# Performance work log

Hardware: AMD Instinct MI355X
Metric: run time of the kernel (lower is better)

Reference implementation:

```python
import jax, jax.numpy as jnp
import numpy as np

N_RAYS, MAX_S, N_VOX, EMB, HID, L_VIEW = 8192, 64, 100000, 32, 128, 4


def view_pe(d):
    # NeRF positional encoding of view dirs: [N,3] -> [N, 3 + 6*L_VIEW]
    freqs = 2.0 ** jnp.arange(L_VIEW, dtype=d.dtype)
    ang = (d[..., None] * freqs).reshape(*d.shape[:-1], -1)  # [N, 3*L]
    return jnp.concatenate([d, jnp.sin(ang), jnp.cos(ang)], -1)


def setup_inputs() -> dict:
    key = jax.random.key(0)
    ks = jax.random.split(key, 16)
    rays_d = jax.random.normal(ks[0], (N_RAYS, 3), dtype=jnp.float32)
    rays_d = rays_d / jnp.linalg.norm(rays_d, axis=-1, keepdims=True)
    pts = jax.random.uniform(ks[1], (N_RAYS, MAX_S, 3), dtype=jnp.float32)
    t_vals = jnp.sort(jax.random.uniform(ks[2], (N_RAYS, MAX_S), dtype=jnp.float32) * 4.0, axis=-1)
    dists = jnp.concatenate([t_vals[:, 1:] - t_vals[:, :-1], jnp.full((N_RAYS, 1), 0.05, jnp.float32)], -1)
    # ragged per-ray sample counts -> -1 padded p2v_idx (as produced by the voxel point sampler)
    counts = jax.random.randint(ks[3], (N_RAYS,), 1, MAX_S + 1)
    ray_hits = jax.random.bernoulli(ks[4], 0.9, (N_RAYS,))
    valid = (jnp.arange(MAX_S)[None, :] < counts[:, None]) & ray_hits[:, None]
    idx = jax.random.randint(ks[5], (N_RAYS, MAX_S), 0, N_VOX)
    p2v_idx = jnp.where(valid, idx, -1).astype(jnp.int32)

    def lin(k, i, o):
        return jax.random.normal(k, (i, o), dtype=jnp.float32) * np.float32(1.0 / np.sqrt(i))

    return dict(
        rays_d=rays_d, pts=pts, t_vals=t_vals, dists=dists,
        p2v_idx=p2v_idx, ray_hits=ray_hits,
        vox_emb=jax.random.normal(ks[6], (N_VOX, EMB), dtype=jnp.float32) * 0.1,
        Wpts=lin(ks[7], 3, EMB),
        W1=lin(ks[8], EMB, HID), b1=jnp.zeros((HID,), jnp.float32),
        W2=lin(ks[9], HID, HID), b2=jnp.zeros((HID,), jnp.float32),
        Wsig=lin(ks[10], HID, 1), bsig=jnp.zeros((1,), jnp.float32),
        Wfeat=lin(ks[11], HID, HID), bfeat=jnp.zeros((HID,), jnp.float32),
        Wc1=lin(ks[12], HID + 3 + 6 * L_VIEW, 64), bc1=jnp.zeros((64,), jnp.float32),
        Wc2=lin(ks[13], 64, 3), bc2=jnp.zeros((3,), jnp.float32),
    )


def reference(rays_d, pts, t_vals, dists, vox_emb, Wpts, W1, b1, W2, b2,
              Wsig, bsig, Wfeat, bfeat, Wc1, bc1, Wc2, bc2, p2v_idx, ray_hits):
    mask = p2v_idx >= 0                                   # [N,S] valid samples (mask_pts)
    idx = jnp.where(mask, p2v_idx, 0)
    # voxel_embedder: per-point voxel embedding gather + positional lift
    ve = vox_emb[idx] + pts @ Wpts                        # [N,S,EMB]
    h = jax.nn.relu(ve @ W1 + b1)
    h = jax.nn.relu(h @ W2 + b2)                          # [N,S,HID]
    sigma = (h @ Wsig + bsig)[..., 0]                     # [N,S]
    feat = h @ Wfeat + bfeat                              # [N,S,HID]
    vemb = view_pe(rays_d)                                # [N,27]
    vemb = jnp.broadcast_to(vemb[:, None, :], (feat.shape[0], feat.shape[1], vemb.shape[-1]))
    c = jax.nn.relu(jnp.concatenate([feat, vemb], -1) @ Wc1 + bc1)
    rgb_raw = c @ Wc2 + bc2                               # [N,S,3]
    # masked_scatter semantics: invalid slots are 0 before the min_color remap
    rgb = (jnp.where(mask[..., None], rgb_raw, 0.0) + 1.0) * 0.5   # min_color = -1
    free_energy = jnp.where(mask, jax.nn.relu(sigma) * dists, 0.0)  # [N,S]
    # volumetric_rendering(with_dist=True)
    shifted = jnp.concatenate([jnp.zeros_like(free_energy[:, :1]), free_energy[:, :-1]], -1)
    T = jnp.exp(-jnp.cumsum(shifted, -1))
    weights = (1.0 - jnp.exp(-free_energy)) * T           # [N,S]
    comp_rgb = jnp.einsum('ns,nsc->nc', weights, rgb)     # [N,3]
    acc = weights.sum(-1)                                 # [N]
    depth = (weights * t_vals).sum(-1)
    disp = 1.0 / jnp.maximum(1e-10, depth / jnp.maximum(acc, 1e-10))
    # fill_in for missed rays (white_bkgd=False -> fill with 0)
    comp_rgb = jnp.where(ray_hits[:, None], comp_rgb, 0.0)
    disp = jnp.where(ray_hits, disp, 0.0)
    acc = jnp.where(ray_hits, acc, 0.0)
    return comp_rgb, disp, acc
```

## Files before the change

kernel.cpp:

```cpp
#include <hip/hip_runtime.h>
#include <stdint.h>


#define NRAYS 8192
#define MAXS  64
#define EMB   32
#define HID   128
#define NPE   27
#define CH    64
#define NPTS  (NRAYS * MAXS)
#define RCAP  16384

#define WS_WCOMB  0
#define WS_WPE    (WS_WCOMB + HID*CH)
#define WS_BCOMB  (WS_WPE + 32*CH)
#define WS_CCINIT (WS_BCOMB + CH)
#define WS_COUNTS (WS_CCINIT + NRAYS*CH)
#define WS_OFFS   (WS_COUNTS + NRAYS)
#define WS_TOTAL  (WS_OFFS + NRAYS)
#define WS_RCNT   (WS_TOTAL + 1)
#define WS_LIST   (WS_TOTAL + 4)
#define WS_PTOUT  (WS_LIST + NPTS)
#define WS_FRAGS  (WS_PTOUT + 4*NPTS)
#define WS_RLIST  (WS_FRAGS + 56*2*64*4)
#define WS_PTSC   (WS_RLIST + RCAP)

typedef __attribute__((ext_vector_type(8))) short bf16x8;
typedef __attribute__((ext_vector_type(4))) float f32x4;
union FI { int i[4]; int4 v; bf16x8 f; };

#define MFMA16(a, b, c) __builtin_amdgcn_mfma_f32_16x16x32_bf16(a, b, c, 0, 0, 0)

__device__ __forceinline__ f32x4 mfma3(bf16x8 ah, bf16x8 al, bf16x8 bh, bf16x8 bl,
                                       f32x4 c) {
  c = MFMA16(al, bh, c);
  c = MFMA16(ah, bl, c);
  c = MFMA16(ah, bh, c);
  return c;
}

__device__ __forceinline__ void split8(const float* x, bf16x8& hi, bf16x8& lo) {
  FI H, L;
#pragma unroll
  for (int r = 0; r < 4; ++r) {
    unsigned u0 = __float_as_uint(x[2 * r]);
    unsigned u1 = __float_as_uint(x[2 * r + 1]);
    unsigned h0 = u0 & 0xffff0000u, h1 = u1 & 0xffff0000u;
    unsigned l0 = __float_as_uint(x[2 * r] - __uint_as_float(h0));
    unsigned l1 = __float_as_uint(x[2 * r + 1] - __uint_as_float(h1));
    H.i[r] = (int)((h0 >> 16) | (h1 & 0xffff0000u));
    L.i[r] = (int)((l0 >> 16) | (l1 & 0xffff0000u));
  }
  hi = H.f; lo = L.f;
}

__device__ __forceinline__ int packword(float v) {
  unsigned u = __float_as_uint(v);
  unsigned hb = u & 0xffff0000u;
  unsigned lb = __float_as_uint(v - __uint_as_float(hb));
  return (int)((u >> 16) | (lb & 0xffff0000u));
}

__device__ __forceinline__ void unpack8(const int* w, bf16x8& hi, bf16x8& lo) {
  FI H, L;
#pragma unroll
  for (int r = 0; r < 4; ++r) {
    unsigned w0 = (unsigned)w[2 * r], w1 = (unsigned)w[2 * r + 1];
    H.i[r] = (int)((w0 & 0xffffu) | (w1 << 16));
    L.i[r] = (int)((w0 >> 16) | (w1 & 0xffff0000u));
  }
  hi = H.f; lo = L.f;
}

__global__ __launch_bounds__(256) void prep_kernel(
    const float* __restrict__ Wfeat, const float* __restrict__ bfeat,
    const float* __restrict__ Wc1, const float* __restrict__ bc1,
    float* __restrict__ ws) {
  int idx = blockIdx.x * 256 + threadIdx.x;
  if (idx < HID * CH) {
    int m = idx >> 6, j = idx & 63;
    float s = 0.f;
    for (int f = 0; f < HID; ++f) s = fmaf(Wfeat[m * HID + f], Wc1[f * CH + j], s);
    ws[WS_WCOMB + idx] = s;
    return;
  }
  idx -= HID * CH;
  if (idx < 32 * CH) {
    int v = idx >> 6, j = idx & 63;
    ws[WS_WPE + idx] = (v < NPE) ? Wc1[(HID + v) * CH + j] : 0.f;
    return;
  }
  idx -= 32 * CH;
  if (idx < CH) {
    float s = bc1[idx];
    for (int f = 0; f < HID; ++f) s = fmaf(bfeat[f], Wc1[f * CH + idx], s);
    ws[WS_BCOMB + idx] = s;
    return;
  }
  idx -= CH;
  if (idx < 2) ((int*)(ws + WS_TOTAL))[idx] = 0;
}

__global__ __launch_bounds__(256) void prep2_kernel(
    const float* __restrict__ W1, const float* __restrict__ W2,
    float* __restrict__ ws) {
  int t = blockIdx.x * 256 + threadIdx.x;
  if (t >= 56 * 64) return;
  const int fid = t >> 6, lane = t & 63;
  const int n16 = lane & 15, quad = lane >> 4;
  float x[8];
  if (fid < 8) {
    const int n = fid * 16 + n16, k0 = quad * 8;
#pragma unroll
    for (int j = 0; j < 8; ++j) x[j] = W1[(k0 + j) * HID + n];
  } else if (fid < 40) {
    const int f = fid - 8, nt = f >> 2, s = f & 3;
    const int n = nt * 16 + n16, k0 = s * 32 + quad * 8;
#pragma unroll
    for (int j = 0; j < 8; ++j) x[j] = W2[(k0 + j) * HID + n];
  } else {
    const int f = fid - 40, nt = f >> 2, s = f & 3;
    const int n = nt * 16 + n16, k0 = s * 32 + quad * 8;
#pragma unroll
    for (int j = 0; j < 8; ++j) x[j] = ws[WS_WCOMB + (k0 + j) * CH + n];
  }
  FI H, L;
#pragma unroll
  for (int r = 0; r < 4; ++r) {
    unsigned u0 = __float_as_uint(x[2 * r]);
    unsigned u1 = __float_as_uint(x[2 * r + 1]);
    unsigned h0 = u0 & 0xffff0000u, h1 = u1 & 0xffff0000u;
    unsigned l0 = __float_as_uint(x[2 * r] - __uint_as_float(h0));
    unsigned l1 = __float_as_uint(x[2 * r + 1] - __uint_as_float(h1));
    H.i[r] = (int)((h0 >> 16) | (h1 & 0xffff0000u));
    L.i[r] = (int)((l0 >> 16) | (l1 & 0xffff0000u));
  }
  int4* o = (int4*)(ws + WS_FRAGS);
  o[(fid * 2 + 0) * 64 + lane] = H.v;
  o[(fid * 2 + 1) * 64 + lane] = L.v;
}

__global__ __launch_bounds__(256) void count_pe_kernel(
    const float* __restrict__ rays_d, const int* __restrict__ p2v,
    float* __restrict__ ws) {
  const int tid = threadIdx.x;
  const int ray = blockIdx.x * 4 + (tid >> 6);
  const int lane = tid & 63;
  const int v = p2v[ray * MAXS + lane];
  const unsigned long long ball = __ballot(v >= 0);
  if (lane == 0) ((int*)(ws + WS_COUNTS))[ray] = __popcll(ball);

  const float d0 = rays_d[ray * 3 + 0];
  const float d1 = rays_d[ray * 3 + 1];
  const float d2 = rays_d[ray * 3 + 2];
  float vemb[NPE];
  vemb[0] = d0; vemb[1] = d1; vemb[2] = d2;
#pragma unroll
  for (int i = 0; i < 3; ++i) {
    const float di = (i == 0) ? d0 : (i == 1) ? d1 : d2;
#pragma unroll
    for (int l = 0; l < 4; ++l) {
      const float ang = di * (float)(1 << l);
      vemb[3 + i * 4 + l] = __sinf(ang);
      vemb[3 + 12 + i * 4 + l] = __cosf(ang);
    }
  }
  float s = ws[WS_BCOMB + lane];
  const float* wpe = ws + WS_WPE;
#pragma unroll
  for (int vv = 0; vv < NPE; ++vv) s = fmaf(vemb[vv], wpe[vv * CH + lane], s);
  ws[WS_CCINIT + ray * CH + lane] = s;
}

__global__ __launch_bounds__(1024) void scan_kernel(float* __restrict__ ws) {
  const int* counts = (const int*)(ws + WS_COUNTS);
  int* offs = (int*)(ws + WS_OFFS);
  int* totalp = (int*)(ws + WS_TOTAL);
  __shared__ int wsum[16];
  const int tid = threadIdx.x;
  const int lane = tid & 63;
  const int base = tid * 8;
  if (tid == 0) ((int*)(ws + WS_RCNT))[0] = 0;
  int c[8], e[8];
  int run = 0;
#pragma unroll
  for (int i = 0; i < 8; ++i) { c[i] = counts[base + i]; e[i] = run; run += c[i]; }
  int inc = run;
#pragma unroll
  for (int off = 1; off < 64; off <<= 1) {
    int u = __shfl_up(inc, off, 64);
    if (lane >= off) inc += u;
  }
  const int wexcl = inc - run;
  if (lane == 63) wsum[tid >> 6] = inc;
  __syncthreads();
  if (tid < 16) {
    int v = wsum[tid];
    int inc2 = v;
#pragma unroll
    for (int off = 1; off < 16; off <<= 1) {
      int u = __shfl_up(inc2, off, 64);
      if (tid >= off) inc2 += u;
    }
    wsum[tid] = inc2 - v;
    if (tid == 15) totalp[0] = inc2;
  }
  __syncthreads();
  const int wbase = wsum[tid >> 6];
#pragma unroll
  for (int i = 0; i < 8; ++i) offs[base + i] = wbase + wexcl + e[i];
}

__global__ __launch_bounds__(256) void list_kernel(
    const int* __restrict__ p2v, const float* __restrict__ pts,
    float* __restrict__ ws) {
  const int tid = threadIdx.x;
  const int ray = blockIdx.x * 4 + (tid >> 6);
  const int lane = tid & 63;
  const int pidx = ray * MAXS + lane;
  const int gidx = p2v[pidx];
  const bool valid = gidx >= 0;
  const unsigned long long ball = __ballot(valid);
  const int rank = __popcll(ball & ((1ull << lane) - 1ull));
  if (valid) {
    const int off = ((const int*)(ws + WS_OFFS))[ray];
    const int slot = off + rank;
    ((int*)(ws + WS_LIST))[slot] = pidx;
    float4 pc;
    pc.x = pts[pidx * 3 + 0];
    pc.y = pts[pidx * 3 + 1];
    pc.z = pts[pidx * 3 + 2];
    pc.w = __int_as_float(gidx);
    ((float4*)(ws + WS_PTSC))[slot] = pc;
  }
}

__device__ __forceinline__ void ve_frag(const float* __restrict__ vox_emb,
                                        const float* __restrict__ Wpts,
                                        float4 pc, int quad,
                                        bf16x8& hi, bf16x8& lo) {
  float x[8];
  const int gidx = __float_as_int(pc.w);
  const float4* vr = (const float4*)vox_emb + gidx * 8 + quad * 2;
  const float4 va = vr[0], vb = vr[1];
  const float px = pc.x, py = pc.y, pz = pc.z;
  const float4* wp = (const float4*)Wpts;
  const float4 wa0 = wp[quad * 2 + 0], wa1 = wp[quad * 2 + 1];
  const float4 wb0 = wp[8 + quad * 2 + 0], wb1 = wp[8 + quad * 2 + 1];
  const float4 wc0 = wp[16 + quad * 2 + 0], wc1 = wp[16 + quad * 2 + 1];
  x[0] = va.x + fmaf(px, wa0.x, fmaf(py, wb0.x, pz * wc0.x));
  x[1] = va.y + fmaf(px, wa0.y, fmaf(py, wb0.y, pz * wc0.y));
  x[2] = va.z + fmaf(px, wa0.z, fmaf(py, wb0.z, pz * wc0.z));
  x[3] = va.w + fmaf(px, wa0.w, fmaf(py, wb0.w, pz * wc0.w));
  x[4] = vb.x + fmaf(px, wa1.x, fmaf(py, wb1.x, pz * wc1.x));
  x[5] = vb.y + fmaf(px, wa1.y, fmaf(py, wb1.y, pz * wc1.y));
  x[6] = vb.z + fmaf(px, wa1.z, fmaf(py, wb1.z, pz * wc1.z));
  x[7] = vb.w + fmaf(px, wa1.w, fmaf(py, wb1.w, pz * wc1.w));
  split8(x, hi, lo);
}

#define LSTRIDE 133

__global__ __launch_bounds__(128, 2) void mlp_mfma(
    const float* __restrict__ vox_emb, const float* __restrict__ Wpts,
    const float* __restrict__ b1, const float* __restrict__ b2,
    const float* __restrict__ Wsig, const float* __restrict__ bsig,
    const float* __restrict__ Wc2, const float* __restrict__ bc2,
    float* __restrict__ ws) {
  __shared__ int alds[64 * LSTRIDE];
  const int tid = threadIdx.x;
  const int wave = tid >> 6, lane = tid & 63;
  const int n16 = lane & 15, quad = lane >> 4;
  const int total = ((const int*)(ws + WS_TOTAL))[0];
  const int base = blockIdx.x * 64 + wave * 32;
  if (base >= total) return;
  const int* list = (const int*)(ws + WS_LIST);
  const int slot0 = min(base + n16, total - 1);
  const int slot1 = min(base + 16 + n16, total - 1);
  const int pidx0 = list[slot0];
  const int pidx1 = list[slot1];
  const float4 pc0 = ((const float4*)(ws + WS_PTSC))[slot0];
  const float4 pc1 = ((const float4*)(ws + WS_PTSC))[slot1];
  const int4* fb = (const int4*)(ws + WS_FRAGS);

  int4 B1f[16];
#pragma unroll
  for (int i = 0; i < 16; ++i) B1f[i] = fb[i * 64 + lane];

  bf16x8 a0h, a0l, a1h, a1l;
  ve_frag(vox_emb, Wpts, pc0, quad, a0h, a0l);
  ve_frag(vox_emb, Wpts, pc1, quad, a1h, a1l);

  int4 BL[2][16];
#pragma unroll
  for (int nt = 0; nt < 8; ++nt) {
    BL[0][2 * nt]     = fb[((8 + nt * 4) * 2 + 0) * 64 + lane];
    BL[0][2 * nt + 1] = fb[((8 + nt * 4) * 2 + 1) * 64 + lane];
  }

  f32x4 h[2][8];
#pragma unroll
  for (int nt = 0; nt < 8; ++nt) {
    const float bb = b1[nt * 16 + n16];
    h[0][nt] = (f32x4){bb, bb, bb, bb};
    h[1][nt] = h[0][nt];
  }
#pragma unroll
  for (int nt = 0; nt < 8; ++nt) {
    FI H, L; H.v = B1f[2 * nt]; L.v = B1f[2 * nt + 1];
    h[0][nt] = mfma3(a0h, a0l, H.f, L.f, h[0][nt]);
    h[1][nt] = mfma3(a1h, a1l, H.f, L.f, h[1][nt]);
  }
#pragma unroll
  for (int mt = 0; mt < 2; ++mt)
#pragma unroll
    for (int nt = 0; nt < 8; ++nt)
#pragma unroll
      for (int r = 0; r < 4; ++r) {
        const float v = fmaxf(h[mt][nt][r], 0.f);
        alds[(wave * 32 + mt * 16 + quad * 4 + r) * LSTRIDE + nt * 16 + n16] = packword(v);
      }

  f32x4 g[2][8];
#pragma unroll
  for (int nt = 0; nt < 8; ++nt) {
    const float bb = b2[nt * 16 + n16];
    g[0][nt] = (f32x4){bb, bb, bb, bb};
    g[1][nt] = g[0][nt];
  }
  const int rb0 = (wave * 32 + n16) * LSTRIDE;
  const int rb1 = rb0 + 16 * LSTRIDE;
#pragma unroll
  for (int s = 0; s < 4; ++s) {
    if (s < 3) {
#pragma unroll
      for (int nt = 0; nt < 8; ++nt) {
        BL[(s + 1) & 1][2 * nt]     = fb[((8 + nt * 4 + s + 1) * 2 + 0) * 64 + lane];
        BL[(s + 1) & 1][2 * nt + 1] = fb[((8 + nt * 4 + s + 1) * 2 + 1) * 64 + lane];
      }
    }
    int w0[8], w1[8];
#pragma unroll
    for (int j = 0; j < 8; ++j) {
      w0[j] = alds[rb0 + s * 32 + quad * 8 + j];
      w1[j] = alds[rb1 + s * 32 + quad * 8 + j];
    }
    bf16x8 A0h, A0l, A1h, A1l;
    unpack8(w0, A0h, A0l);
    unpack8(w1, A1h, A1l);
#pragma unroll
    for (int nt = 0; nt < 8; ++nt) {
      FI H, L; H.v = BL[s & 1][2 * nt]; L.v = BL[s & 1][2 * nt + 1];
      g[0][nt] = mfma3(A0h, A0l, H.f, L.f, g[0][nt]);
      g[1][nt] = mfma3(A1h, A1l, H.f, L.f, g[1][nt]);
    }
  }

  int pm[2][4];
#pragma unroll
  for (int mt = 0; mt < 2; ++mt)
#pragma unroll
    for (int r = 0; r < 4; ++r)
      pm[mt][r] = __shfl(mt ? pidx1 : pidx0, quad * 4 + r, 64);
  int4 BC[2][8];
#pragma unroll
  for (int nt = 0; nt < 4; ++nt) {
    BC[0][2 * nt]     = fb[((40 + nt * 4) * 2 + 0) * 64 + lane];
    BC[0][2 * nt + 1] = fb[((40 + nt * 4) * 2 + 1) * 64 + lane];
  }
  f32x4 cacc[2][4];
#pragma unroll
  for (int mt = 0; mt < 2; ++mt)
#pragma unroll
    for (int nt = 0; nt < 4; ++nt)
#pragma unroll
      for (int r = 0; r < 4; ++r)
        cacc[mt][nt][r] = ws[WS_CCINIT + (pm[mt][r] >> 6) * CH + nt * 16 + n16];

  float sg[2][4] = {{0.f, 0.f, 0.f, 0.f}, {0.f, 0.f, 0.f, 0.f}};
#pragma unroll
  for (int nt = 0; nt < 8; ++nt) {
    const float sv = Wsig[nt * 16 + n16];
#pragma unroll
    for (int mt = 0; mt < 2; ++mt)
#pragma unroll
      for (int r = 0; r < 4; ++r) {
        const float v = fmaxf(g[mt][nt][r], 0.f);
        sg[mt][r] = fmaf(v, sv, sg[mt][r]);
        alds[(wave * 32 + mt * 16 + quad * 4 + r) * LSTRIDE + nt * 16 + n16] = packword(v);
      }
  }
#pragma unroll
  for (int mask = 1; mask < 16; mask <<= 1)
#pragma unroll
    for (int mt = 0; mt < 2; ++mt)
#pragma unroll
      for (int r = 0; r < 4; ++r) sg[mt][r] += __shfl_xor(sg[mt][r], mask, 64);

#pragma unroll
  for (int s = 0; s < 4; ++s) {
    if (s < 3) {
#pragma unroll
      for (int nt = 0; nt < 4; ++nt) {
        BC[(s + 1) & 1][2 * nt]     = fb[((40 + nt * 4 + s + 1) * 2 + 0) * 64 + lane];
        BC[(s + 1) & 1][2 * nt + 1] = fb[((40 + nt * 4 + s + 1) * 2 + 1) * 64 + lane];
      }
    }
    int w0[8], w1[8];
#pragma unroll
    for (int j = 0; j < 8; ++j) {
      w0[j] = alds[rb0 + s * 32 + quad * 8 + j];
      w1[j] = alds[rb1 + s * 32 + quad * 8 + j];
    }
    bf16x8 A0h, A0l, A1h, A1l;
    unpack8(w0, A0h, A0l);
    unpack8(w1, A1h, A1l);
#pragma unroll
    for (int nt = 0; nt < 4; ++nt) {
      FI H, L; H.v = BC[s & 1][2 * nt]; L.v = BC[s & 1][2 * nt + 1];
      cacc[0][nt] = mfma3(A0h, A0l, H.f, L.f, cacc[0][nt]);
      cacc[1][nt] = mfma3(A1h, A1l, H.f, L.f, cacc[1][nt]);
    }
  }

  float cr[2][3][4];
#pragma unroll
  for (int mt = 0; mt < 2; ++mt)
#pragma unroll
    for (int c = 0; c < 3; ++c)
#pragma unroll
      for (int r = 0; r < 4; ++r) cr[mt][c][r] = 0.f;
#pragma unroll
  for (int nt = 0; nt < 4; ++nt) {
    const int j = nt * 16 + n16;
    const float w0 = Wc2[j * 3 + 0], w1c = Wc2[j * 3 + 1], w2c = Wc2[j * 3 + 2];
#pragma unroll
    for (int mt = 0; mt < 2; ++mt)
#pragma unroll
      for (int r = 0; r < 4; ++r) {
        const float cv = fmaxf(cacc[mt][nt][r], 0.f);
        cr[mt][0][r] = fmaf(cv, w0, cr[mt][0][r]);
        cr[mt][1][r] = fmaf(cv, w1c, cr[mt][1][r]);
        cr[mt][2][r] = fmaf(cv, w2c, cr[mt][2][r]);
      }
  }
#pragma unroll
  for (int mask = 1; mask < 16; mask <<= 1)
#pragma unroll
    for (int mt = 0; mt < 2; ++mt)
#pragma unroll
      for (int c = 0; c < 3; ++c)
#pragma unroll
        for (int r = 0; r < 4; ++r) cr[mt][c][r] += __shfl_xor(cr[mt][c][r], mask, 64);

  if (n16 == 0) {
    const float bs = bsig[0];
    const float bcr = bc2[0], bcg = bc2[1], bcb = bc2[2];
#pragma unroll
    for (int mt = 0; mt < 2; ++mt)
#pragma unroll
      for (int r = 0; r < 4; ++r) {
        const int m = mt * 16 + quad * 4 + r;
        if (base + m < total) {
          const int pid = pm[mt][r];
          const float sig = sg[mt][r] + bs;
          ((float4*)(ws + WS_PTOUT))[pid] =
              make_float4(sig, cr[mt][0][r] + bcr, cr[mt][1][r] + bcg, cr[mt][2][r] + bcb);
          if (fabsf(sig) < 0.006f) {
            const int ri = atomicAdd((int*)(ws + WS_RCNT), 1);
            if (ri < RCAP) ((int*)(ws + WS_RLIST))[ri] = pid;
          }
        }
      }
  }
}

__device__ __forceinline__ float wave_sum(float v) {
#pragma unroll
  for (int off = 32; off > 0; off >>= 1) v += __shfl_down(v, off, 64);
  return v;
}

__global__ __launch_bounds__(256) void repair_kernel(
    const float* __restrict__ pts, const int* __restrict__ p2v,
    const float* __restrict__ vox_emb, const float* __restrict__ Wpts,
    const float* __restrict__ W1, const float* __restrict__ b1,
    const float* __restrict__ W2, const float* __restrict__ b2,
    const float* __restrict__ Wsig, const float* __restrict__ bsig,
    float* __restrict__ ws) {
  __shared__ float h1s[4][HID];
  const int wv = threadIdx.x >> 6, lane = threadIdx.x & 63;
  const int cnt = min(((const int*)(ws + WS_RCNT))[0], RCAP);
  const int nw = gridDim.x * 4;
  for (int i = blockIdx.x * 4 + wv; i < cnt; i += nw) {
    const int pidx = ((const int*)(ws + WS_RLIST))[i];
    const int gidx = p2v[pidx];
    const float px = pts[pidx * 3 + 0];
    const float py = pts[pidx * 3 + 1];
    const float pz = pts[pidx * 3 + 2];
    float ve[EMB];
#pragma unroll
    for (int e = 0; e < EMB; ++e)
      ve[e] = vox_emb[gidx * EMB + e] +
              fmaf(px, Wpts[e], fmaf(py, Wpts[EMB + e], pz * Wpts[2 * EMB + e]));
    float s0 = b1[lane], s1 = b1[lane + 64];
#pragma unroll
    for (int k = 0; k < EMB; ++k) {
      const float x = ve[k];
      s0 = fmaf(x, W1[k * HID + lane], s0);
      s1 = fmaf(x, W1[k * HID + lane + 64], s1);
    }
    h1s[wv][lane] = fmaxf(s0, 0.f);
    h1s[wv][lane + 64] = fmaxf(s1, 0.f);
    float t0 = b2[lane], t1 = b2[lane + 64];
    for (int k = 0; k < HID; ++k) {
      const float x = h1s[wv][k];
      t0 = fmaf(x, W2[k * HID + lane], t0);
      t1 = fmaf(x, W2[k * HID + lane + 64], t1);
    }
    float sp = fmaf(fmaxf(t0, 0.f), Wsig[lane], fmaxf(t1, 0.f) * Wsig[lane + 64]);
    sp = wave_sum(sp);
    if (lane == 0) ws[WS_PTOUT + 4 * pidx + 0] = sp + bsig[0];
  }
}

__device__ __forceinline__ float wave_prefix_excl(float v, int lane) {
  float inc = v;
#pragma unroll
  for (int off = 1; off < 64; off <<= 1) {
    float u = __shfl_up(inc, off, 64);
    if (lane >= off) inc += u;
  }
  return inc - v;
}

__global__ __launch_bounds__(256) void render_kernel(
    const float* __restrict__ t_vals, const float* __restrict__ dists,
    const int* __restrict__ p2v, const float* __restrict__ ws,
    float* __restrict__ out_rgb, float* __restrict__ out_disp,
    float* __restrict__ out_acc) {
  const int tid = threadIdx.x;
  const int ray = blockIdx.x * 4 + (tid >> 6);
  const int lane = tid & 63;
  const int pidx = ray * MAXS + lane;

  const int vidx = p2v[pidx];
  const bool hit = (__shfl(vidx, 0, 64) >= 0);
  if (!hit) {
    if (lane < 3) out_rgb[ray * 3 + lane] = 0.f;
    if (lane == 0) { out_disp[ray] = 0.f; out_acc[ray] = 0.f; }
    return;
  }
  const bool valid = vidx >= 0;

  const float4 pv = ((const float4*)(ws + WS_PTOUT))[pidx];
  const float fe = valid ? fmaxf(pv.x, 0.f) * dists[pidx] : 0.f;
  const float pref = wave_prefix_excl(fe, lane);
  const float T = __expf(-pref);
  const float w = (1.f - __expf(-fe)) * T;
  const float tv = t_vals[pidx];

  const float crgb0 = wave_sum(w * (pv.y + 1.f) * 0.5f);
  const float crgb1 = wave_sum(w * (pv.z + 1.f) * 0.5f);
  const float crgb2 = wave_sum(w * (pv.w + 1.f) * 0.5f);
  const float accs = wave_sum(w);
  const float depth = wave_sum(w * tv);

  if (lane == 0) {
    out_rgb[ray * 3 + 0] = crgb0;
    out_rgb[ray * 3 + 1] = crgb1;
    out_rgb[ray * 3 + 2] = crgb2;
    const float disp = 1.f / fmaxf(1e-10f, depth / fmaxf(accs, 1e-10f));
    out_disp[ray] = disp;
    out_acc[ray] = accs;
  }
}

extern "C" void kernel_launch(void* const* d_in, const int* in_sizes, int n_in,
                              void* d_out, int out_size, void* d_ws, size_t ws_size,
                              hipStream_t stream) {
  const float* rays_d  = (const float*)d_in[0];
  const float* pts     = (const float*)d_in[1];
  const float* t_vals  = (const float*)d_in[2];
  const float* dists   = (const float*)d_in[3];
  const int*   p2v     = (const int*)d_in[4];
  const float* vox_emb = (const float*)d_in[6];
  const float* Wpts    = (const float*)d_in[7];
  const float* W1      = (const float*)d_in[8];
  const float* b1      = (const float*)d_in[9];
  const float* W2      = (const float*)d_in[10];
  const float* b2      = (const float*)d_in[11];
  const float* Wsig    = (const float*)d_in[12];
  const float* bsig    = (const float*)d_in[13];
  const float* Wfeat   = (const float*)d_in[14];
  const float* bfeat   = (const float*)d_in[15];
  const float* Wc1     = (const float*)d_in[16];
  const float* bc1     = (const float*)d_in[17];
  const float* Wc2     = (const float*)d_in[18];
  const float* bc2     = (const float*)d_in[19];

  float* ws = (float*)d_ws;
  float* out = (float*)d_out;
  float* out_rgb = out;
  float* out_disp = out + NRAYS * 3;
  float* out_acc = out + NRAYS * 4;

  hipLaunchKernelGGL(prep_kernel, dim3(41), dim3(256), 0, stream,
                     Wfeat, bfeat, Wc1, bc1, ws);
  hipLaunchKernelGGL(prep2_kernel, dim3(14), dim3(256), 0, stream, W1, W2, ws);
  hipLaunchKernelGGL(count_pe_kernel, dim3(NRAYS / 4), dim3(256), 0, stream,
                     rays_d, p2v, ws);
  hipLaunchKernelGGL(scan_kernel, dim3(1), dim3(1024), 0, stream, ws);
  hipLaunchKernelGGL(list_kernel, dim3(NRAYS / 4), dim3(256), 0, stream,
                     p2v, pts, ws);
  hipLaunchKernelGGL(mlp_mfma, dim3(NPTS / 64), dim3(128), 0, stream,
                     vox_emb, Wpts, b1, b2, Wsig, bsig, Wc2, bc2, ws);
  hipLaunchKernelGGL(repair_kernel, dim3(128), dim3(256), 0, stream,
                     pts, p2v, vox_emb, Wpts, W1, b1, W2, b2, Wsig, bsig, ws);
  hipLaunchKernelGGL(render_kernel, dim3(NRAYS / 4), dim3(256), 0, stream,
                     t_vals, dists, p2v, ws, out_rgb, out_disp, out_acc);
}
```

Measured before the change: 260.5 us.

## Fuse sigma repair into render, merge prep kernels, halve MLP tile per wave

The separate repair kernel and its atomic-appended repair list are removed. Near-zero sigma points are now recomputed in fp32 inside the render kernel, serially per wave via a ballot loop. The two prep kernels are merged, so the combined Wfeat·Wc1 weight is computed inline when building fragments. The MFMA MLP now processes 16 points per wave instead of 32, with half the LDS and launch bounds raised to 4 blocks per SM for more occupancy. The trade-off is less weight-fragment reuse per wave, more blocks, and redundant per-thread dot products in prep.

```diff
diff --git a/kernel.cpp b/kernel.cpp
--- a/kernel.cpp
+++ b/kernel.cpp
@@ -9,27 +9,24 @@
 #define NPE   27
 #define CH    64
 #define NPTS  (NRAYS * MAXS)
-#define RCAP  16384
-
-#define WS_WCOMB  0
-#define WS_WPE    (WS_WCOMB + HID*CH)
+
+#define WS_WPE    0
 #define WS_BCOMB  (WS_WPE + 32*CH)
 #define WS_CCINIT (WS_BCOMB + CH)
 #define WS_COUNTS (WS_CCINIT + NRAYS*CH)
 #define WS_OFFS   (WS_COUNTS + NRAYS)
 #define WS_TOTAL  (WS_OFFS + NRAYS)
-#define WS_RCNT   (WS_TOTAL + 1)
 #define WS_LIST   (WS_TOTAL + 4)
 #define WS_PTOUT  (WS_LIST + NPTS)
 #define WS_FRAGS  (WS_PTOUT + 4*NPTS)
-#define WS_RLIST  (WS_FRAGS + 56*2*64*4)
-#define WS_PTSC   (WS_RLIST + RCAP)
+#define WS_PTSC   (WS_FRAGS + 56*2*64*4)
 
 typedef __attribute__((ext_vector_type(8))) short bf16x8;
 typedef __attribute__((ext_vector_type(4))) float f32x4;
 union FI { int i[4]; int4 v; bf16x8 f; };
 
 #define MFMA16(a, b, c) __builtin_amdgcn_mfma_f32_16x16x32_bf16(a, b, c, 0, 0, 0)
+#define LSTRIDE 133
 
 __device__ __forceinline__ f32x4 mfma3(bf16x8 ah, bf16x8 al, bf16x8 bh, bf16x8 bl,
                                        f32x4 c) {
@@ -72,19 +69,28 @@
   hi = H.f; lo = L.f;
 }
 
+__device__ __forceinline__ float wave_sum(float v) {
+#pragma unroll
+  for (int off = 32; off > 0; off >>= 1) v += __shfl_down(v, off, 64);
+  return v;
+}
+
+__device__ __forceinline__ float wave_prefix_excl(float v, int lane) {
+  float inc = v;
+#pragma unroll
+  for (int off = 1; off < 64; off <<= 1) {
+    float u = __shfl_up(inc, off, 64);
+    if (lane >= off) inc += u;
+  }
+  return inc - v;
+}
+
 __global__ __launch_bounds__(256) void prep_kernel(
+    const float* __restrict__ W1, const float* __restrict__ W2,
     const float* __restrict__ Wfeat, const float* __restrict__ bfeat,
     const float* __restrict__ Wc1, const float* __restrict__ bc1,
     float* __restrict__ ws) {
   int idx = blockIdx.x * 256 + threadIdx.x;
-  if (idx < HID * CH) {
-    int m = idx >> 6, j = idx & 63;
-    float s = 0.f;
-    for (int f = 0; f < HID; ++f) s = fmaf(Wfeat[m * HID + f], Wc1[f * CH + j], s);
-    ws[WS_WCOMB + idx] = s;
-    return;
-  }
-  idx -= HID * CH;
   if (idx < 32 * CH) {
     int v = idx >> 6, j = idx & 63;
     ws[WS_WPE + idx] = (v < NPE) ? Wc1[(HID + v) * CH + j] : 0.f;
@@ -98,15 +104,8 @@
     return;
   }
   idx -= CH;
-  if (idx < 2) ((int*)(ws + WS_TOTAL))[idx] = 0;
-}
-
-__global__ __launch_bounds__(256) void prep2_kernel(
-    const float* __restrict__ W1, const float* __restrict__ W2,
-    float* __restrict__ ws) {
-  int t = blockIdx.x * 256 + threadIdx.x;
-  if (t >= 56 * 64) return;
-  const int fid = t >> 6, lane = t & 63;
+  if (idx >= 56 * 64) return;
+  const int fid = idx >> 6, lane = idx & 63;
   const int n16 = lane & 15, quad = lane >> 4;
   float x[8];
   if (fid < 8) {
@@ -122,7 +121,12 @@
     const int f = fid - 40, nt = f >> 2, s = f & 3;
     const int n = nt * 16 + n16, k0 = s * 32 + quad * 8;
 #pragma unroll
-    for (int j = 0; j < 8; ++j) x[j] = ws[WS_WCOMB + (k0 + j) * CH + n];
+    for (int j = 0; j < 8; ++j) {
+      float sum = 0.f;
+      const float* wf = Wfeat + (k0 + j) * HID;
+      for (int ff = 0; ff < HID; ++ff) sum = fmaf(wf[ff], Wc1[ff * CH + n], sum);
+      x[j] = sum;
+    }
   }
   FI H, L;
 #pragma unroll
@@ -180,7 +184,6 @@
   const int tid = threadIdx.x;
   const int lane = tid & 63;
   const int base = tid * 8;
-  if (tid == 0) ((int*)(ws + WS_RCNT))[0] = 0;
   int c[8], e[8];
   int run = 0;
 #pragma unroll
@@ -259,37 +262,31 @@
   split8(x, hi, lo);
 }
 
-#define LSTRIDE 133
-
-__global__ __launch_bounds__(128, 2) void mlp_mfma(
+__global__ __launch_bounds__(128, 4) void mlp_mfma(
     const float* __restrict__ vox_emb, const float* __restrict__ Wpts,
     const float* __restrict__ b1, const float* __restrict__ b2,
     const float* __restrict__ Wsig, const float* __restrict__ bsig,
     const float* __restrict__ Wc2, const float* __restrict__ bc2,
     float* __restrict__ ws) {
-  __shared__ int alds[64 * LSTRIDE];
+  __shared__ int alds[32 * LSTRIDE];
   const int tid = threadIdx.x;
   const int wave = tid >> 6, lane = tid & 63;
   const int n16 = lane & 15, quad = lane >> 4;
   const int total = ((const int*)(ws + WS_TOTAL))[0];
-  const int base = blockIdx.x * 64 + wave * 32;
+  const int base = blockIdx.x * 32 + wave * 16;
   if (base >= total) return;
   const int* list = (const int*)(ws + WS_LIST);
   const int slot0 = min(base + n16, total - 1);
-  const int slot1 = min(base + 16 + n16, total - 1);
   const int pidx0 = list[slot0];
-  const int pidx1 = list[slot1];
   const float4 pc0 = ((const float4*)(ws + WS_PTSC))[slot0];
-  const float4 pc1 = ((const float4*)(ws + WS_PTSC))[slot1];
   const int4* fb = (const int4*)(ws + WS_FRAGS);
 
   int4 B1f[16];
 #pragma unroll
   for (int i = 0; i < 16; ++i) B1f[i] = fb[i * 64 + lane];
 
-  bf16x8 a0h, a0l, a1h, a1l;
+  bf16x8 a0h, a0l;
   ve_frag(vox_emb, Wpts, pc0, quad, a0h, a0l);
-  ve_frag(vox_emb, Wpts, pc1, quad, a1h, a1l);
 
   int4 BL[2][16];
 #pragma unroll
@@ -298,38 +295,32 @@
     BL[0][2 * nt + 1] = fb[((8 + nt * 4) * 2 + 1) * 64 + lane];
   }
 
-  f32x4 h[2][8];
+  f32x4 h[8];
 #pragma unroll
   for (int nt = 0; nt < 8; ++nt) {
     const float bb = b1[nt * 16 + n16];
-    h[0][nt] = (f32x4){bb, bb, bb, bb};
-    h[1][nt] = h[0][nt];
+    h[nt] = (f32x4){bb, bb, bb, bb};
   }
 #pragma unroll
   for (int nt = 0; nt < 8; ++nt) {
     FI H, L; H.v = B1f[2 * nt]; L.v = B1f[2 * nt + 1];
-    h[0][nt] = mfma3(a0h, a0l, H.f, L.f, h[0][nt]);
-    h[1][nt] = mfma3(a1h, a1l, H.f, L.f, h[1][nt]);
-  }
-#pragma unroll
-  for (int mt = 0; mt < 2; ++mt)
-#pragma unroll
-    for (int nt = 0; nt < 8; ++nt)
-#pragma unroll
-      for (int r = 0; r < 4; ++r) {
-        const float v = fmaxf(h[mt][nt][r], 0.f);
-        alds[(wave * 32 + mt * 16 + quad * 4 + r) * LSTRIDE + nt * 16 + n16] = packword(v);
-      }
-
-  f32x4 g[2][8];
+    h[nt] = mfma3(a0h, a0l, H.f, L.f, h[nt]);
+  }
+#pragma unroll
+  for (int nt = 0; nt < 8; ++nt)
+#pragma unroll
+    for (int r = 0; r < 4; ++r) {
+      const float v = fmaxf(h[nt][r], 0.f);
+      alds[(wave * 16 + quad * 4 + r) * LSTRIDE + nt * 16 + n16] = packword(v);
+    }
+
+  f32x4 g[8];
 #pragma unroll
   for (int nt = 0; nt < 8; ++nt) {
     const float bb = b2[nt * 16 + n16];
-    g[0][nt] = (f32x4){bb, bb, bb, bb};
-    g[1][nt] = g[0][nt];
-  }
-  const int rb0 = (wave * 32 + n16) * LSTRIDE;
-  const int rb1 = rb0 + 16 * LSTRIDE;
+    g[nt] = (f32x4){bb, bb, bb, bb};
+  }
+  const int rb0 = (wave * 16 + n16) * LSTRIDE;
 #pragma unroll
   for (int s = 0; s < 4; ++s) {
     if (s < 3) {
@@ -339,63 +330,49 @@
         BL[(s + 1) & 1][2 * nt + 1] = fb[((8 + nt * 4 + s + 1) * 2 + 1) * 64 + lane];
       }
     }
-    int w0[8], w1[8];
-#pragma unroll
-    for (int j = 0; j < 8; ++j) {
-      w0[j] = alds[rb0 + s * 32 + quad * 8 + j];
-      w1[j] = alds[rb1 + s * 32 + quad * 8 + j];
-    }
-    bf16x8 A0h, A0l, A1h, A1l;
+    int w0[8];
+#pragma unroll
+    for (int j = 0; j < 8; ++j) w0[j] = alds[rb0 + s * 32 + quad * 8 + j];
+    bf16x8 A0h, A0l;
     unpack8(w0, A0h, A0l);
-    unpack8(w1, A1h, A1l);
 #pragma unroll
     for (int nt = 0; nt < 8; ++nt) {
       FI H, L; H.v = BL[s & 1][2 * nt]; L.v = BL[s & 1][2 * nt + 1];
-      g[0][nt] = mfma3(A0h, A0l, H.f, L.f, g[0][nt]);
-      g[1][nt] = mfma3(A1h, A1l, H.f, L.f, g[1][nt]);
-    }
-  }
-
-  int pm[2][4];
-#pragma unroll
-  for (int mt = 0; mt < 2; ++mt)
-#pragma unroll
-    for (int r = 0; r < 4; ++r)
-      pm[mt][r] = __shfl(mt ? pidx1 : pidx0, quad * 4 + r, 64);
+      g[nt] = mfma3(A0h, A0l, H.f, L.f, g[nt]);
+    }
+  }
+
+  int pm[4];
+#pragma unroll
+  for (int r = 0; r < 4; ++r) pm[r] = __shfl(pidx0, quad * 4 + r, 64);
   int4 BC[2][8];
 #pragma unroll
   for (int nt = 0; nt < 4; ++nt) {
     BC[0][2 * nt]     = fb[((40 + nt * 4) * 2 + 0) * 64 + lane];
     BC[0][2 * nt + 1] = fb[((40 + nt * 4) * 2 + 1) * 64 + lane];
   }
-  f32x4 cacc[2][4];
-#pragma unroll
-  for (int mt = 0; mt < 2; ++mt)
-#pragma unroll
-    for (int nt = 0; nt < 4; ++nt)
-#pragma unroll
-      for (int r = 0; r < 4; ++r)
-        cacc[mt][nt][r] = ws[WS_CCINIT + (pm[mt][r] >> 6) * CH + nt * 16 + n16];
-
-  float sg[2][4] = {{0.f, 0.f, 0.f, 0.f}, {0.f, 0.f, 0.f, 0.f}};
+  f32x4 cacc[4];
+#pragma unroll
+  for (int nt = 0; nt < 4; ++nt)
+#pragma unroll
+    for (int r = 0; r < 4; ++r)
+      cacc[nt][r] = ws[WS_CCINIT + (pm[r] >> 6) * CH + nt * 16 + n16];
+
+  float sg[4] = {0.f, 0.f, 0.f, 0.f};
 #pragma unroll
   for (int nt = 0; nt < 8; ++nt) {
     const float sv = Wsig[nt * 16 + n16];
 #pragma unroll
-    for (int mt = 0; mt < 2; ++mt)
-#pragma unroll
-      for (int r = 0; r < 4; ++r) {
-        const float v = fmaxf(g[mt][nt][r], 0.f);
-        sg[mt][r] = fmaf(v, sv, sg[mt][r]);
-        alds[(wave * 32 + mt * 16 + quad * 4 + r) * LSTRIDE + nt * 16 + n16] = packword(v);
-      }
+    for (int r = 0; r < 4; ++r) {
+      const float v = fmaxf(g[nt][r], 0.f);
+      sg[r] = fmaf(v, sv, sg[r]);
+      alds[(wave * 16 + quad * 4 + r) * LSTRIDE + nt * 16 + n16] = packword(v);
+    }
   }
 #pragma unroll
   for (int mask = 1; mask < 16; mask <<= 1)
 #pragma unroll
-    for (int mt = 0; mt < 2; ++mt)
-#pragma unroll
-      for (int r = 0; r < 4; ++r) sg[mt][r] += __shfl_xor(sg[mt][r], mask, 64);
+    for (int r = 0; r < 4; ++r) sg[r] += __shfl_xor(sg[r], mask, 64);
 
 #pragma unroll
   for (int s = 0; s < 4; ++s) {
@@ -406,141 +383,70 @@
         BC[(s + 1) & 1][2 * nt + 1] = fb[((40 + nt * 4 + s + 1) * 2 + 1) * 64 + lane];
       }
     }
-    int w0[8], w1[8];
-#pragma unroll
-    for (int j = 0; j < 8; ++j) {
-      w0[j] = alds[rb0 + s * 32 + quad * 8 + j];
-      w1[j] = alds[rb1 + s * 32 + quad * 8 + j];
-    }
-    bf16x8 A0h, A0l, A1h, A1l;
+    int w0[8];
+#pragma unroll
+    for (int j = 0; j < 8; ++j) w0[j] = alds[rb0 + s * 32 + quad * 8 + j];
+    bf16x8 A0h, A0l;
     unpack8(w0, A0h, A0l);
-    unpack8(w1, A1h, A1l);
 #pragma unroll
     for (int nt = 0; nt < 4; ++nt) {
       FI H, L; H.v = BC[s & 1][2 * nt]; L.v = BC[s & 1][2 * nt + 1];
-      cacc[0][nt] = mfma3(A0h, A0l, H.f, L.f, cacc[0][nt]);
-      cacc[1][nt] = mfma3(A1h, A1l, H.f, L.f, cacc[1][nt]);
-    }
-  }
-
-  float cr[2][3][4];
-#pragma unroll
-  for (int mt = 0; mt < 2; ++mt)
-#pragma unroll
-    for (int c = 0; c < 3; ++c)
-#pragma unroll
-      for (int r = 0; r < 4; ++r) cr[mt][c][r] = 0.f;
+      cacc[nt] = mfma3(A0h, A0l, H.f, L.f, cacc[nt]);
+    }
+  }
+
+  float cr[3][4];
+#pragma unroll
+  for (int c = 0; c < 3; ++c)
+#pragma unroll
+    for (int r = 0; r < 4; ++r) cr[c][r] = 0.f;
 #pragma unroll
   for (int nt = 0; nt < 4; ++nt) {
     const int j = nt * 16 + n16;
     const float w0 = Wc2[j * 3 + 0], w1c = Wc2[j * 3 + 1], w2c = Wc2[j * 3 + 2];
 #pragma unroll
-    for (int mt = 0; mt < 2; ++mt)
-#pragma unroll
-      for (int r = 0; r < 4; ++r) {
-        const float cv = fmaxf(cacc[mt][nt][r], 0.f);
-        cr[mt][0][r] = fmaf(cv, w0, cr[mt][0][r]);
-        cr[mt][1][r] = fmaf(cv, w1c, cr[mt][1][r]);
-        cr[mt][2][r] = fmaf(cv, w2c, cr[mt][2][r]);
-      }
+    for (int r = 0; r < 4; ++r) {
+      const float cv = fmaxf(cacc[nt][r], 0.f);
+      cr[0][r] = fmaf(cv, w0, cr[0][r]);
+      cr[1][r] = fmaf(cv, w1c, cr[1][r]);
+      cr[2][r] = fmaf(cv, w2c, cr[2][r]);
+    }
   }
 #pragma unroll
   for (int mask = 1; mask < 16; mask <<= 1)
 #pragma unroll
-    for (int mt = 0; mt < 2; ++mt)
-#pragma unroll
-      for (int c = 0; c < 3; ++c)
-#pragma unroll
-        for (int r = 0; r < 4; ++r) cr[mt][c][r] += __shfl_xor(cr[mt][c][r], mask, 64);
+    for (int c = 0; c < 3; ++c)
+#pragma unroll
+      for (int r = 0; r < 4; ++r) cr[c][r] += __shfl_xor(cr[c][r], mask, 64);
 
   if (n16 == 0) {
     const float bs = bsig[0];
     const float bcr = bc2[0], bcg = bc2[1], bcb = bc2[2];
 #pragma unroll
-    for (int mt = 0; mt < 2; ++mt)
-#pragma unroll
-      for (int r = 0; r < 4; ++r) {
-        const int m = mt * 16 + quad * 4 + r;
-        if (base + m < total) {
-          const int pid = pm[mt][r];
-          const float sig = sg[mt][r] + bs;
-          ((float4*)(ws + WS_PTOUT))[pid] =
-              make_float4(sig, cr[mt][0][r] + bcr, cr[mt][1][r] + bcg, cr[mt][2][r] + bcb);
-          if (fabsf(sig) < 0.006f) {
-            const int ri = atomicAdd((int*)(ws + WS_RCNT), 1);
-            if (ri < RCAP) ((int*)(ws + WS_RLIST))[ri] = pid;
-          }
-        }
+    for (int r = 0; r < 4; ++r) {
+      const int m = quad * 4 + r;
+      if (base + m < total) {
+        ((float4*)(ws + WS_PTOUT))[pm[r]] =
+            make_float4(sg[r] + bs, cr[0][r] + bcr, cr[1][r] + bcg, cr[2][r] + bcb);
       }
-  }
-}
-
-__device__ __forceinline__ float wave_sum(float v) {
-#pragma unroll
-  for (int off = 32; off > 0; off >>= 1) v += __shfl_down(v, off, 64);
-  return v;
-}
-
-__global__ __launch_bounds__(256) void repair_kernel(
-    const float* __restrict__ pts, const int* __restrict__ p2v,
+    }
+  }
+}
+
+__global__ __launch_bounds__(256) void render_kernel(
+    const float* __restrict__ t_vals, const float* __restrict__ dists,
+    const int* __restrict__ p2v, const float* __restrict__ pts,
     const float* __restrict__ vox_emb, const float* __restrict__ Wpts,
     const float* __restrict__ W1, const float* __restrict__ b1,
     const float* __restrict__ W2, const float* __restrict__ b2,
     const float* __restrict__ Wsig, const float* __restrict__ bsig,
-    float* __restrict__ ws) {
-  __shared__ float h1s[4][HID];
-  const int wv = threadIdx.x >> 6, lane = threadIdx.x & 63;
-  const int cnt = min(((const int*)(ws + WS_RCNT))[0], RCAP);
-  const int nw = gridDim.x * 4;
-  for (int i = blockIdx.x * 4 + wv; i < cnt; i += nw) {
-    const int pidx = ((const int*)(ws + WS_RLIST))[i];
-    const int gidx = p2v[pidx];
-    const float px = pts[pidx * 3 + 0];
-    const float py = pts[pidx * 3 + 1];
-    const float pz = pts[pidx * 3 + 2];
-    float ve[EMB];
-#pragma unroll
-    for (int e = 0; e < EMB; ++e)
-      ve[e] = vox_emb[gidx * EMB + e] +
-              fmaf(px, Wpts[e], fmaf(py, Wpts[EMB + e], pz * Wpts[2 * EMB + e]));
-    float s0 = b1[lane], s1 = b1[lane + 64];
-#pragma unroll
-    for (int k = 0; k < EMB; ++k) {
-      const float x = ve[k];
-      s0 = fmaf(x, W1[k * HID + lane], s0);
-      s1 = fmaf(x, W1[k * HID + lane + 64], s1);
-    }
-    h1s[wv][lane] = fmaxf(s0, 0.f);
-    h1s[wv][lane + 64] = fmaxf(s1, 0.f);
-    float t0 = b2[lane], t1 = b2[lane + 64];
-    for (int k = 0; k < HID; ++k) {
-      const float x = h1s[wv][k];
-      t0 = fmaf(x, W2[k * HID + lane], t0);
-      t1 = fmaf(x, W2[k * HID + lane + 64], t1);
-    }
-    float sp = fmaf(fmaxf(t0, 0.f), Wsig[lane], fmaxf(t1, 0.f) * Wsig[lane + 64]);
-    sp = wave_sum(sp);
-    if (lane == 0) ws[WS_PTOUT + 4 * pidx + 0] = sp + bsig[0];
-  }
-}
-
-__device__ __forceinline__ float wave_prefix_excl(float v, int lane) {
-  float inc = v;
-#pragma unroll
-  for (int off = 1; off < 64; off <<= 1) {
-    float u = __shfl_up(inc, off, 64);
-    if (lane >= off) inc += u;
-  }
-  return inc - v;
-}
-
-__global__ __launch_bounds__(256) void render_kernel(
-    const float* __restrict__ t_vals, const float* __restrict__ dists,
-    const int* __restrict__ p2v, const float* __restrict__ ws,
+    const float* __restrict__ ws,
     float* __restrict__ out_rgb, float* __restrict__ out_disp,
     float* __restrict__ out_acc) {
+  __shared__ float h1s[4][HID];
   const int tid = threadIdx.x;
-  const int ray = blockIdx.x * 4 + (tid >> 6);
+  const int wv = tid >> 6;
+  const int ray = blockIdx.x * 4 + wv;
   const int lane = tid & 63;
   const int pidx = ray * MAXS + lane;
 
@@ -554,7 +460,45 @@
   const bool valid = vidx >= 0;
 
   const float4 pv = ((const float4*)(ws + WS_PTOUT))[pidx];
-  const float fe = valid ? fmaxf(pv.x, 0.f) * dists[pidx] : 0.f;
+  float sigx = pv.x;
+
+  unsigned long long need = __ballot(valid && fabsf(sigx) < 0.006f);
+  while (need) {
+    const int fl = (int)(__ffsll((long long)need) - 1);
+    need &= need - 1;
+    const int rpidx = ray * MAXS + fl;
+    const int gidx = __shfl(vidx, fl, 64);
+    const float px = pts[rpidx * 3 + 0];
+    const float py = pts[rpidx * 3 + 1];
+    const float pz = pts[rpidx * 3 + 2];
+    float ve[EMB];
+#pragma unroll
+    for (int e = 0; e < EMB; ++e)
+      ve[e] = vox_emb[gidx * EMB + e] +
+              fmaf(px, Wpts[e], fmaf(py, Wpts[EMB + e], pz * Wpts[2 * EMB + e]));
+    float s0 = b1[lane], s1 = b1[lane + 64];
+#pragma unroll
+    for (int k = 0; k < EMB; ++k) {
+      const float x = ve[k];
+      s0 = fmaf(x, W1[k * HID + lane], s0);
+      s1 = fmaf(x, W1[k * HID + lane + 64], s1);
+    }
+    h1s[wv][lane] = fmaxf(s0, 0.f);
+    h1s[wv][lane + 64] = fmaxf(s1, 0.f);
+    float t0 = b2[lane], t1 = b2[lane + 64];
+#pragma unroll 1
+    for (int k = 0; k < HID; ++k) {
+      const float x = h1s[wv][k];
+      t0 = fmaf(x, W2[k * HID + lane], t0);
+      t1 = fmaf(x, W2[k * HID + lane + 64], t1);
+    }
+    float sp = fmaf(fmaxf(t0, 0.f), Wsig[lane], fmaxf(t1, 0.f) * Wsig[lane + 64]);
+    sp = wave_sum(sp);
+    sp = __shfl(sp, 0, 64) + bsig[0];
+    if (lane == fl) sigx = sp;
+  }
+
+  const float fe = valid ? fmaxf(sigx, 0.f) * dists[pidx] : 0.f;
   const float pref = wave_prefix_excl(fe, lane);
   const float T = __expf(-pref);
   const float w = (1.f - __expf(-fe)) * T;
@@ -605,18 +549,17 @@
   float* out_disp = out + NRAYS * 3;
   float* out_acc = out + NRAYS * 4;
 
-  hipLaunchKernelGGL(prep_kernel, dim3(41), dim3(256), 0, stream,
-                     Wfeat, bfeat, Wc1, bc1, ws);
-  hipLaunchKernelGGL(prep2_kernel, dim3(14), dim3(256), 0, stream, W1, W2, ws);
+  hipLaunchKernelGGL(prep_kernel, dim3(23), dim3(256), 0, stream,
+                     W1, W2, Wfeat, bfeat, Wc1, bc1, ws);
   hipLaunchKernelGGL(count_pe_kernel, dim3(NRAYS / 4), dim3(256), 0, stream,
                      rays_d, p2v, ws);
   hipLaunchKernelGGL(scan_kernel, dim3(1), dim3(1024), 0, stream, ws);
   hipLaunchKernelGGL(list_kernel, dim3(NRAYS / 4), dim3(256), 0, stream,
                      p2v, pts, ws);
-  hipLaunchKernelGGL(mlp_mfma, dim3(NPTS / 64), dim3(128), 0, stream,
+  hipLaunchKernelGGL(mlp_mfma, dim3(NPTS / 32), dim3(128), 0, stream,
                      vox_emb, Wpts, b1, b2, Wsig, bsig, Wc2, bc2, ws);
-  hipLaunchKernelGGL(repair_kernel, dim3(128), dim3(256), 0, stream,
-                     pts, p2v, vox_emb, Wpts, W1, b1, W2, b2, Wsig, bsig, ws);
   hipLaunchKernelGGL(render_kernel, dim3(NRAYS / 4), dim3(256), 0, stream,
-                     t_vals, dists, p2v, ws, out_rgb, out_disp, out_acc);
-}
+                     t_vals, dists, p2v, pts, vox_emb, Wpts,
+                     W1, b1, W2, b2, Wsig, bsig, ws,
+                     out_rgb, out_disp, out_acc);
+}
```

Result: slower. 361.5 us (+38.8%).
